# Kernel optimization log

Measured on AMD Instinct MI355X. Metric: run time of the kernel, lower is better.

The kernel has to match this reference:

```python
import jax, jax.numpy as jnp
import numpy as np

NUM_JOINTS = 24
PARENTS = np.array([-1, 0, 0, 0, 1, 2, 3, 4, 5, 6, 7, 8, 9, 9, 9, 12, 13, 14, 16, 17, 18, 19, 20, 21])
SENSOR_IDX = np.array([0, 4, 5, 15, 18, 19])          # pelvis, knees, head, elbows (6 IMUs)
IGNORED_IDX = np.array([7, 8, 10, 11, 20, 21, 22, 23])  # ankles, feet, wrists, hands
REDUCED_IDX = np.array([1, 2, 3, 6, 9, 12, 13, 14, 16, 17])  # 10 reduced joints
IGNORED_PARENTS = PARENTS[IGNORED_IDX]


def rotation_6d_to_matrix(d6):
    # pytorch3d convention: rows b1, b2, b3
    a1, a2 = d6[..., :3], d6[..., 3:]
    b1 = a1 / jnp.linalg.norm(a1, axis=-1, keepdims=True)
    b2 = a2 - jnp.sum(b1 * a2, axis=-1, keepdims=True) * b1
    b2 = b2 / jnp.linalg.norm(b2, axis=-1, keepdims=True)
    b3 = jnp.cross(b1, b2)
    return jnp.stack([b1, b2, b3], axis=-2)


def matrix_to_quaternion(m):
    m00, m01, m02 = m[..., 0, 0], m[..., 0, 1], m[..., 0, 2]
    m10, m11, m12 = m[..., 1, 0], m[..., 1, 1], m[..., 1, 2]
    m20, m21, m22 = m[..., 2, 0], m[..., 2, 1], m[..., 2, 2]
    q_abs = jnp.sqrt(jnp.maximum(jnp.stack([
        1.0 + m00 + m11 + m22,
        1.0 + m00 - m11 - m22,
        1.0 - m00 + m11 - m22,
        1.0 - m00 - m11 + m22], axis=-1), 0.0))
    quat_by_rijk = jnp.stack([
        jnp.stack([q_abs[..., 0] ** 2, m21 - m12, m02 - m20, m10 - m01], axis=-1),
        jnp.stack([m21 - m12, q_abs[..., 1] ** 2, m10 + m01, m02 + m20], axis=-1),
        jnp.stack([m02 - m20, m10 + m01, q_abs[..., 2] ** 2, m12 + m21], axis=-1),
        jnp.stack([m10 - m01, m20 + m02, m21 + m12, q_abs[..., 3] ** 2], axis=-1),
    ], axis=-2)
    quat_candidates = quat_by_rijk / (2.0 * jnp.maximum(q_abs[..., None], 0.1))
    idx = jnp.argmax(q_abs, axis=-1)
    return jnp.take_along_axis(quat_candidates, idx[..., None, None], axis=-2)[..., 0, :]


def quaternion_to_axis_angle(q):
    norms = jnp.linalg.norm(q[..., 1:], axis=-1, keepdims=True)
    half_angles = jnp.arctan2(norms, q[..., :1])
    angles = 2.0 * half_angles
    small = jnp.abs(angles) < 1e-6
    safe_angles = jnp.where(small, 1.0, angles)
    sin_half_over_angle = jnp.where(small, 0.5 - angles * angles / 48.0,
                                    jnp.sin(half_angles) / safe_angles)
    return q[..., 1:] / sin_half_over_angle


def matrix_to_axis_angle(m):
    return quaternion_to_axis_angle(matrix_to_quaternion(m))


def setup_inputs() -> dict:
    key = jax.random.key(0)
    k1, k2 = jax.random.split(key)
    B, T = 1024, 256
    glb_reduced_6d = jax.random.normal(k1, (B, T, len(REDUCED_IDX), 6), dtype=jnp.float32)
    orientation_6d = jax.random.normal(k2, (B, T, len(SENSOR_IDX), 6), dtype=jnp.float32)
    return {"glb_reduced_6d": glb_reduced_6d, "orientation_6d": orientation_6d}


def reference(glb_reduced_6d, orientation_6d):
    B, T = glb_reduced_6d.shape[:2]
    BT = B * T
    dtype = glb_reduced_6d.dtype
    glb6 = glb_reduced_6d.reshape(BT, len(REDUCED_IDX), 6)
    ori6 = orientation_6d.reshape(BT, len(SENSOR_IDX), 6)

    orientation = rotation_6d_to_matrix(ori6)          # [BT, 6, 3, 3]
    root = orientation[:, 0]                           # [BT, 3, 3]
    reduced_rot = rotation_6d_to_matrix(glb6)          # [BT, 10, 3, 3]

    # _reduced_glb_6d_to_full_glb_mat
    reduced_glb = jnp.einsum('bij,brjk->brik', root, reduced_rot)
    ori_glb = orientation.at[:, 1:].set(jnp.einsum('bij,bsjk->bsik', root, orientation[:, 1:]))
    eye = jnp.eye(3, dtype=dtype)
    full = jnp.broadcast_to(eye, (BT, NUM_JOINTS, 3, 3))
    full = full.at[:, REDUCED_IDX].set(reduced_glb)
    full = full.at[:, SENSOR_IDX].set(ori_glb)
    # torch advanced-index assignment: RHS gathered from pre-update values
    full = full.at[:, IGNORED_IDX].set(full[:, IGNORED_PARENTS])

    # _global2local: local_i = R_parent(i)^T @ R_i (vectorized over static parent gather)
    parent_rot = full[:, PARENTS[1:]]                  # [BT, 23, 3, 3]
    local_rest = jnp.einsum('bjki,bjkl->bjil', parent_rot, full[:, 1:])
    local = jnp.concatenate([full[:, :1], local_rest], axis=1)
    local = local.at[:, IGNORED_IDX].set(eye)

    pose_aa = matrix_to_axis_angle(local)              # [BT, 24, 3]
    return pose_aa.reshape(B, T, NUM_JOINTS, 3)
```

## Files before the change

kernel.cpp:

```cpp
#include <hip/hip_runtime.h>
#include <math.h>


__device__ __forceinline__ void rot6d_v(float2 u0, float2 u1, float2 u2, float M[3][3]) {
    float a1x = u0.x, a1y = u0.y, a1z = u1.x;
    float a2x = u1.y, a2y = u2.x, a2z = u2.y;
    float r1 = __builtin_amdgcn_rsqf(a1x * a1x + a1y * a1y + a1z * a1z);
    float b1x = a1x * r1, b1y = a1y * r1, b1z = a1z * r1;
    float dt = b1x * a2x + b1y * a2y + b1z * a2z;
    float c2x = a2x - dt * b1x, c2y = a2y - dt * b1y, c2z = a2z - dt * b1z;
    float r2 = __builtin_amdgcn_rsqf(c2x * c2x + c2y * c2y + c2z * c2z);
    float b2x = c2x * r2, b2y = c2y * r2, b2z = c2z * r2;
    float b3x = b1y * b2z - b1z * b2y;
    float b3y = b1z * b2x - b1x * b2z;
    float b3z = b1x * b2y - b1y * b2x;
    M[0][0] = b1x; M[0][1] = b1y; M[0][2] = b1z;
    M[1][0] = b2x; M[1][1] = b2y; M[1][2] = b2z;
    M[2][0] = b3x; M[2][1] = b3y; M[2][2] = b3z;
}

__device__ __forceinline__ void matTmul(const float A[3][3], const float B[3][3], float C[3][3]) {
#pragma unroll
    for (int i = 0; i < 3; ++i)
#pragma unroll
        for (int j = 0; j < 3; ++j)
            C[i][j] = A[0][i] * B[0][j] + A[1][i] * B[1][j] + A[2][i] * B[2][j];
}

__device__ __forceinline__ float atan2_pos(float y, float x) {
    float ax = fabsf(x);
    float mx = fmaxf(y, ax);
    float mn = fminf(y, ax);
    float a = mn * __builtin_amdgcn_rcpf(mx);
    float s = a * a;
    float p = -0.0040540580f;
    p = fmaf(p, s, 0.0218612288f);
    p = fmaf(p, s, -0.0559098861f);
    p = fmaf(p, s, 0.0964200441f);
    p = fmaf(p, s, -0.1390853351f);
    p = fmaf(p, s, 0.1994653599f);
    p = fmaf(p, s, -0.3332985605f);
    p = fmaf(p, s, 0.9999993329f);
    float r = p * a;
    r = (y > ax) ? (1.5707963268f - r) : r;
    r = (x < 0.f) ? (3.1415926536f - r) : r;
    return r;
}

__device__ __forceinline__ void mat2aa(const float m[3][3], float* __restrict__ outp) {
    float m00 = m[0][0], m01 = m[0][1], m02 = m[0][2];
    float m10 = m[1][0], m11 = m[1][1], m12 = m[1][2];
    float m20 = m[2][0], m21 = m[2][1], m22 = m[2][2];
    float t0 = fmaxf(1.f + m00 + m11 + m22, 0.f);
    float t1 = fmaxf(1.f + m00 - m11 - m22, 0.f);
    float t2 = fmaxf(1.f - m00 + m11 - m22, 0.f);
    float t3 = fmaxf(1.f - m00 - m11 + m22, 0.f);
    int idx = 0;
    float bt = t0;
    if (t1 > bt) { bt = t1; idx = 1; }
    if (t2 > bt) { bt = t2; idx = 2; }
    if (t3 > bt) { bt = t3; idx = 3; }
    float best = __builtin_amdgcn_sqrtf(bt);
    float s1 = m21 - m12, s2 = m02 - m20, s3 = m10 - m01;
    float p1 = m10 + m01, p2 = m02 + m20, p3 = m12 + m21;
    float w = (idx == 0) ? bt : (idx == 1) ? s1 : (idx == 2) ? s2 : s3;
    float x = (idx == 0) ? s1 : (idx == 1) ? bt : (idx == 2) ? p1 : p2;
    float y = (idx == 0) ? s2 : (idx == 1) ? p1 : (idx == 2) ? bt : p3;
    float z = (idx == 0) ? s3 : (idx == 1) ? p2 : (idx == 2) ? p3 : bt;
    float inv = 0.5f * __builtin_amdgcn_rcpf(fmaxf(best, 0.1f));
    w *= inv; x *= inv; y *= inv; z *= inv;
    float n = __builtin_amdgcn_sqrtf(x * x + y * y + z * z);
    float half = atan2_pos(n, w);
    float angle = 2.f * half;
    float inv_sh = (angle < 1e-6f) ? 2.f : angle * __builtin_amdgcn_rcpf(n);
    outp[0] = x * inv_sh;
    outp[1] = y * inv_sh;
    outp[2] = z * inv_sh;
}

__global__ __launch_bounds__(1024) void pose_kernel(const float* __restrict__ glb,
                                                    const float* __restrict__ ori,
                                                    float* __restrict__ out, int BT) {
    int tid = blockIdx.x * 1024 + threadIdx.x;
    unsigned e = (unsigned)tid >> 4;
    if (e >= (unsigned)BT) return;
    int l = tid & 15;

    const unsigned long long OUT3_LO = 0x1B120F0C09060300ULL;
    const unsigned long long OUT3_HI = 0x393633302D2A2724ULL;
    const unsigned long long SRCJ_LO = 0x0403121102010010ULL;
    const unsigned long long SRCJ_HI = 0x1514090813070605ULL;
    const unsigned long long PL_LO   = 0x0603020100000000ULL;
    const unsigned long long PL_HI   = 0x0D0C0A0908070707ULL;
    const unsigned long long IGN3    = 0x45423F3C211E1815ULL;

    int sh = (l & 7) * 8;
    unsigned out3 = (unsigned)(((l < 8 ? OUT3_LO : OUT3_HI) >> sh) & 0xFF);
    unsigned srcj = (unsigned)(((l < 8 ? SRCJ_LO : SRCJ_HI) >> sh) & 0xFF);
    int pl = (int)(((l < 8 ? PL_LO : PL_HI) >> sh) & 0xFF);

    unsigned row6 = (srcj & 15) * 6;
    unsigned goff = __umul24(e, 60u) + row6;
    unsigned ooff = __umul24(e, 36u) + row6;
    const float* src = (srcj & 0x10) ? (ori + ooff) : (glb + goff);
    const float2* s2 = (const float2*)src;
    float2 u0 = s2[0], u1 = s2[1], u2 = s2[2];

    float X[3][3];
    rot6d_v(u0, u1, u2, X);

    float Xp[3][3];
    {
        const float* xf = &X[0][0];
        float* pf = &Xp[0][0];
#pragma unroll
        for (int k = 0; k < 9; ++k) pf[k] = __shfl(xf[k], pl, 16);
    }

    float L[3][3];
    matTmul(Xp, X, L);
#pragma unroll
    for (int i = 0; i < 3; ++i)
#pragma unroll
        for (int j = 0; j < 3; ++j)
            L[i][j] = (l < 4) ? X[i][j] : L[i][j];

    float* oute = out + __umul24(e, 72u);
    mat2aa(L, oute + out3);

    if (l < 8) {
        unsigned z = (unsigned)((IGN3 >> sh) & 0xFF);
        float* zp = oute + z;
        zp[0] = 0.f; zp[1] = 0.f; zp[2] = 0.f;
    }
}

extern "C" void kernel_launch(void* const* d_in, const int* in_sizes, int n_in,
                              void* d_out, int out_size, void* d_ws, size_t ws_size,
                              hipStream_t stream) {
    const float* glb = (const float*)d_in[0];
    const float* ori = (const float*)d_in[1];
    float* out = (float*)d_out;
    int BT = in_sizes[0] / 60;
    long long threads = (long long)BT * 16;
    int block = 1024;
    int grid = (int)((threads + block - 1) / block);
    pose_kernel<<<grid, block, 0, stream>>>(glb, ori, out, BT);
}
```

Before: 151.2 us.

## Stage per-element outputs in LDS and write coalesced nontemporal vector stores

Each thread now writes its 3-float axis-angle result and the zeroed ignored-joint entries into a shared-memory tile covering 16 elements. After a barrier, the block writes the tile out as contiguous 16-byte nontemporal stores. This replaces scattered 4-byte global stores with fully coalesced vector writes. Block size drops from 1024 to 256 threads, and the change adds a block-wide sync and an LDS round trip.

```diff
diff --git a/kernel.cpp b/kernel.cpp
--- a/kernel.cpp
+++ b/kernel.cpp
@@ -1,6 +1,8 @@
 #include <hip/hip_runtime.h>
 #include <math.h>
 
+
+typedef float f32x4 __attribute__((ext_vector_type(4)));
 
 __device__ __forceinline__ void rot6d_v(float2 u0, float2 u1, float2 u2, float M[3][3]) {
     float a1x = u0.x, a1y = u0.y, a1z = u1.x;
@@ -78,13 +80,17 @@
     outp[2] = z * inv_sh;
 }
 
-__global__ __launch_bounds__(1024) void pose_kernel(const float* __restrict__ glb,
-                                                    const float* __restrict__ ori,
-                                                    float* __restrict__ out, int BT) {
-    int tid = blockIdx.x * 1024 + threadIdx.x;
-    unsigned e = (unsigned)tid >> 4;
-    if (e >= (unsigned)BT) return;
-    int l = tid & 15;
+__global__ __launch_bounds__(256) void pose_kernel(const float* __restrict__ glb,
+                                                   const float* __restrict__ ori,
+                                                   float* __restrict__ out, int BT) {
+    __shared__ float lds[16 * 72];
+
+    int t = threadIdx.x;
+    int base = blockIdx.x * 16;
+    int eloc = t >> 4;
+    int l = t & 15;
+    int g = base + eloc;
+    unsigned e = (unsigned)((g < BT) ? g : (BT - 1));
 
     const unsigned long long OUT3_LO = 0x1B120F0C09060300ULL;
     const unsigned long long OUT3_HI = 0x393633302D2A2724ULL;
@@ -100,9 +106,8 @@
     int pl = (int)(((l < 8 ? PL_LO : PL_HI) >> sh) & 0xFF);
 
     unsigned row6 = (srcj & 15) * 6;
-    unsigned goff = __umul24(e, 60u) + row6;
-    unsigned ooff = __umul24(e, 36u) + row6;
-    const float* src = (srcj & 0x10) ? (ori + ooff) : (glb + goff);
+    const float* src = (srcj & 0x10) ? (ori + __umul24(e, 36u) + row6)
+                                     : (glb + __umul24(e, 60u) + row6);
     const float2* s2 = (const float2*)src;
     float2 u0 = s2[0], u1 = s2[1], u2 = s2[2];
 
@@ -125,14 +130,22 @@
         for (int j = 0; j < 3; ++j)
             L[i][j] = (l < 4) ? X[i][j] : L[i][j];
 
-    float* oute = out + __umul24(e, 72u);
-    mat2aa(L, oute + out3);
-
+    float* op = lds + eloc * 72;
+    mat2aa(L, op + out3);
     if (l < 8) {
         unsigned z = (unsigned)((IGN3 >> sh) & 0xFF);
-        float* zp = oute + z;
+        float* zp = op + z;
         zp[0] = 0.f; zp[1] = 0.f; zp[2] = 0.f;
     }
+    __syncthreads();
+
+    int nelem = BT - base;
+    if (nelem > 16) nelem = 16;
+    int nf4 = nelem * 18;
+    const f32x4* l4 = (const f32x4*)lds;
+    f32x4* g4 = (f32x4*)(out + (size_t)base * 72);
+    for (int i = t; i < nf4; i += 256)
+        __builtin_nontemporal_store(l4[i], g4 + i);
 }
 
 extern "C" void kernel_launch(void* const* d_in, const int* in_sizes, int n_in,
@@ -142,8 +155,6 @@
     const float* ori = (const float*)d_in[1];
     float* out = (float*)d_out;
     int BT = in_sizes[0] / 60;
-    long long threads = (long long)BT * 16;
-    int block = 1024;
-    int grid = (int)((threads + block - 1) / block);
-    pose_kernel<<<grid, block, 0, stream>>>(glb, ori, out, BT);
+    int grid = (BT + 15) / 16;
+    pose_kernel<<<grid, 256, 0, stream>>>(glb, ori, out, BT);
 }
```

Result: no change. 151.7 us (+0.3%).

## Compose local rotations via quaternions instead of 3x3 matrix products

Applied to the files above, without the earlier changes.

Each lane now converts its global rotation matrix to a quaternion first. It then shuffles 4 quaternion components from the parent lane instead of 9 matrix entries, and forms the relative rotation with a conjugate quaternion product. Sign canonicalization (flipping so the largest-magnitude component is positive) mimics the original matrix-to-quaternion branch selection. This cuts shuffle traffic and arithmetic, but results may differ slightly numerically from the matrix path. The block size also drops from 1024 to 256.

```diff
diff --git a/kernel.cpp b/kernel.cpp
--- a/kernel.cpp
+++ b/kernel.cpp
@@ -19,12 +19,29 @@
     M[2][0] = b3x; M[2][1] = b3y; M[2][2] = b3z;
 }
 
-__device__ __forceinline__ void matTmul(const float A[3][3], const float B[3][3], float C[3][3]) {
-#pragma unroll
-    for (int i = 0; i < 3; ++i)
-#pragma unroll
-        for (int j = 0; j < 3; ++j)
-            C[i][j] = A[0][i] * B[0][j] + A[1][i] * B[1][j] + A[2][i] * B[2][j];
+__device__ __forceinline__ void mat2quat(const float m[3][3],
+                                         float& qw, float& qx, float& qy, float& qz) {
+    float m00 = m[0][0], m01 = m[0][1], m02 = m[0][2];
+    float m10 = m[1][0], m11 = m[1][1], m12 = m[1][2];
+    float m20 = m[2][0], m21 = m[2][1], m22 = m[2][2];
+    float t0 = fmaxf(1.f + m00 + m11 + m22, 0.f);
+    float t1 = fmaxf(1.f + m00 - m11 - m22, 0.f);
+    float t2 = fmaxf(1.f - m00 + m11 - m22, 0.f);
+    float t3 = fmaxf(1.f - m00 - m11 + m22, 0.f);
+    int idx = 0;
+    float bt = t0;
+    if (t1 > bt) { bt = t1; idx = 1; }
+    if (t2 > bt) { bt = t2; idx = 2; }
+    if (t3 > bt) { bt = t3; idx = 3; }
+    float best = __builtin_amdgcn_sqrtf(bt);
+    float s1 = m21 - m12, s2 = m02 - m20, s3 = m10 - m01;
+    float p1 = m10 + m01, p2 = m02 + m20, p3 = m12 + m21;
+    float w = (idx == 0) ? bt : (idx == 1) ? s1 : (idx == 2) ? s2 : s3;
+    float x = (idx == 0) ? s1 : (idx == 1) ? bt : (idx == 2) ? p1 : p2;
+    float y = (idx == 0) ? s2 : (idx == 1) ? p1 : (idx == 2) ? bt : p3;
+    float z = (idx == 0) ? s3 : (idx == 1) ? p2 : (idx == 2) ? p3 : bt;
+    float inv = 0.5f * __builtin_amdgcn_rcpf(fmaxf(best, 0.1f));
+    qw = w * inv; qx = x * inv; qy = y * inv; qz = z * inv;
 }
 
 __device__ __forceinline__ float atan2_pos(float y, float x) {
@@ -47,41 +64,10 @@
     return r;
 }
 
-__device__ __forceinline__ void mat2aa(const float m[3][3], float* __restrict__ outp) {
-    float m00 = m[0][0], m01 = m[0][1], m02 = m[0][2];
-    float m10 = m[1][0], m11 = m[1][1], m12 = m[1][2];
-    float m20 = m[2][0], m21 = m[2][1], m22 = m[2][2];
-    float t0 = fmaxf(1.f + m00 + m11 + m22, 0.f);
-    float t1 = fmaxf(1.f + m00 - m11 - m22, 0.f);
-    float t2 = fmaxf(1.f - m00 + m11 - m22, 0.f);
-    float t3 = fmaxf(1.f - m00 - m11 + m22, 0.f);
-    int idx = 0;
-    float bt = t0;
-    if (t1 > bt) { bt = t1; idx = 1; }
-    if (t2 > bt) { bt = t2; idx = 2; }
-    if (t3 > bt) { bt = t3; idx = 3; }
-    float best = __builtin_amdgcn_sqrtf(bt);
-    float s1 = m21 - m12, s2 = m02 - m20, s3 = m10 - m01;
-    float p1 = m10 + m01, p2 = m02 + m20, p3 = m12 + m21;
-    float w = (idx == 0) ? bt : (idx == 1) ? s1 : (idx == 2) ? s2 : s3;
-    float x = (idx == 0) ? s1 : (idx == 1) ? bt : (idx == 2) ? p1 : p2;
-    float y = (idx == 0) ? s2 : (idx == 1) ? p1 : (idx == 2) ? bt : p3;
-    float z = (idx == 0) ? s3 : (idx == 1) ? p2 : (idx == 2) ? p3 : bt;
-    float inv = 0.5f * __builtin_amdgcn_rcpf(fmaxf(best, 0.1f));
-    w *= inv; x *= inv; y *= inv; z *= inv;
-    float n = __builtin_amdgcn_sqrtf(x * x + y * y + z * z);
-    float half = atan2_pos(n, w);
-    float angle = 2.f * half;
-    float inv_sh = (angle < 1e-6f) ? 2.f : angle * __builtin_amdgcn_rcpf(n);
-    outp[0] = x * inv_sh;
-    outp[1] = y * inv_sh;
-    outp[2] = z * inv_sh;
-}
-
-__global__ __launch_bounds__(1024) void pose_kernel(const float* __restrict__ glb,
-                                                    const float* __restrict__ ori,
-                                                    float* __restrict__ out, int BT) {
-    int tid = blockIdx.x * 1024 + threadIdx.x;
+__global__ __launch_bounds__(256) void pose_kernel(const float* __restrict__ glb,
+                                                   const float* __restrict__ ori,
+                                                   float* __restrict__ out, int BT) {
+    int tid = blockIdx.x * 256 + threadIdx.x;
     unsigned e = (unsigned)tid >> 4;
     if (e >= (unsigned)BT) return;
     int l = tid & 15;
@@ -100,33 +86,55 @@
     int pl = (int)(((l < 8 ? PL_LO : PL_HI) >> sh) & 0xFF);
 
     unsigned row6 = (srcj & 15) * 6;
-    unsigned goff = __umul24(e, 60u) + row6;
-    unsigned ooff = __umul24(e, 36u) + row6;
-    const float* src = (srcj & 0x10) ? (ori + ooff) : (glb + goff);
+    const float* src = (srcj & 0x10) ? (ori + __umul24(e, 36u) + row6)
+                                     : (glb + __umul24(e, 60u) + row6);
     const float2* s2 = (const float2*)src;
     float2 u0 = s2[0], u1 = s2[1], u2 = s2[2];
 
     float X[3][3];
     rot6d_v(u0, u1, u2, X);
 
-    float Xp[3][3];
+    float qw, qx, qy, qz;
+    mat2quat(X, qw, qx, qy, qz);
+
+    float pw = __shfl(qw, pl, 16);
+    float px = __shfl(qx, pl, 16);
+    float py = __shfl(qy, pl, 16);
+    float pz = __shfl(qz, pl, 16);
+
+    float rw = pw * qw + px * qx + py * qy + pz * qz;
+    float rx = pw * qx - px * qw - py * qz + pz * qy;
+    float ry = pw * qy + px * qz - py * qw - pz * qx;
+    float rz = pw * qz - px * qy + py * qx - pz * qw;
+    bool direct = (l < 4);
+    rw = direct ? qw : rw;
+    rx = direct ? qx : rx;
+    ry = direct ? qy : ry;
+    rz = direct ? qz : rz;
+
     {
-        const float* xf = &X[0][0];
-        float* pf = &Xp[0][0];
-#pragma unroll
-        for (int k = 0; k < 9; ++k) pf[k] = __shfl(xf[k], pl, 16);
+        float aw = fabsf(rw), ax = fabsf(rx), ay = fabsf(ry), az = fabsf(rz);
+        float m = aw; float c = rw;
+        if (ax > m) { m = ax; c = rx; }
+        if (ay > m) { m = ay; c = ry; }
+        if (az > m) { m = az; c = rz; }
+        unsigned sgn = __float_as_uint(c) & 0x80000000u;
+        rw = __uint_as_float(__float_as_uint(rw) ^ sgn);
+        rx = __uint_as_float(__float_as_uint(rx) ^ sgn);
+        ry = __uint_as_float(__float_as_uint(ry) ^ sgn);
+        rz = __uint_as_float(__float_as_uint(rz) ^ sgn);
     }
 
-    float L[3][3];
-    matTmul(Xp, X, L);
-#pragma unroll
-    for (int i = 0; i < 3; ++i)
-#pragma unroll
-        for (int j = 0; j < 3; ++j)
-            L[i][j] = (l < 4) ? X[i][j] : L[i][j];
+    float n = __builtin_amdgcn_sqrtf(rx * rx + ry * ry + rz * rz);
+    float half = atan2_pos(n, rw);
+    float angle = 2.f * half;
+    float inv_sh = (angle < 1e-6f) ? 2.f : angle * __builtin_amdgcn_rcpf(n);
 
     float* oute = out + __umul24(e, 72u);
-    mat2aa(L, oute + out3);
+    float* op = oute + out3;
+    op[0] = rx * inv_sh;
+    op[1] = ry * inv_sh;
+    op[2] = rz * inv_sh;
 
     if (l < 8) {
         unsigned z = (unsigned)((IGN3 >> sh) & 0xFF);
@@ -143,7 +151,7 @@
     float* out = (float*)d_out;
     int BT = in_sizes[0] / 60;
     long long threads = (long long)BT * 16;
-    int block = 1024;
+    int block = 256;
     int grid = (int)((threads + block - 1) / block);
     pose_kernel<<<grid, block, 0, stream>>>(glb, ori, out, BT);
 }
```

Result: no change. 149.6 us (-1.1%).
